# Kernel tuning notes

Measured on AMD Instinct MI355X. Metric: run time of the kernel, lower is better.

## Reference

```python
import jax, jax.numpy as jnp
import numpy as np

ROUTING_ITERATIONS = 3

def squash(x, axis=-1):
    # norm_sq/(1+norm_sq) * x/norm, equation 1 of the CapsNet paper
    norm_sq = jnp.sum(x * x, axis=axis, keepdims=True)
    norm = jnp.sqrt(norm_sq)
    return norm_sq / (1.0 + norm_sq) * (x / norm)

def setup_inputs() -> dict:
    key = jax.random.key(0)
    k1, k2 = jax.random.split(key)
    B, IC, IH, OC, OH = 64, 2048, 16, 64, 32
    input_capsules = jax.random.normal(k1, (B, IC, IH), dtype=jnp.float32)
    # scale weight so U entries are O(1) (sum over in_hid=16)
    W = jax.random.normal(k2, (IC, IH, OC, OH), dtype=jnp.float32) * (1.0 / np.sqrt(IH))
    return {"input_capsules": input_capsules, "W": W}

def reference(input_capsules, W):
    # U[b,i,o,j] = sum_h x[b,i,h] * W[i,h,o,j]
    U = jnp.einsum('bih,ihoj->bioj', input_capsules, W)
    b, in_caps, out_caps, out_hid = U.shape
    Blog = jnp.zeros((b, in_caps, out_caps), dtype=U.dtype)

    def body(Blog, _):
        C = jax.nn.softmax(Blog, axis=-1)            # [b,i,o]
        S = jnp.einsum('bio,bioh->boh', C, U)        # [b,o,h]
        V = squash(S, axis=-1)                       # [b,o,h]
        Blog = Blog + jnp.einsum('bioh,boh->bio', U, V)
        return Blog, V

    _, Vs = jax.lax.scan(body, Blog, None, length=ROUTING_ITERATIONS)
    return Vs[-1]
```

## Files before the change

### kernel.cpp

```cpp
#include <hip/hip_runtime.h>
#include <hip/hip_bf16.h>
#include <cstdint>
#include <cstddef>

constexpr int B_SZ = 64, IC = 2048, IH = 16, OC = 64, OH = 32;
constexpr int NN = OC * OH;
constexpr int ICHUNK = 32;
constexpr int NCHUNK = IC / ICHUNK;
constexpr int BTILE = 16;

typedef __attribute__((ext_vector_type(8))) short bf16x8;
typedef __attribute__((ext_vector_type(4))) float f32x4;

constexpr int F_Z = 0;
constexpr int F_W = 64;
constexpr int F_WBUF = 65536;
constexpr int BL_ROW = 68;
constexpr int F_BL = F_W + 2 * F_WBUF;
constexpr int F_C = F_BL + 16 * BL_ROW * 4;
constexpr int F_SMEM = F_C + 16 * BL_ROW * 4;

__device__ __forceinline__ unsigned short f2bf(float f) {
    unsigned u = __float_as_uint(f);
    u += 0x7fffu + ((u >> 16) & 1u);
    return (unsigned short)(u >> 16);
}
__device__ __forceinline__ float bf_lo(unsigned u) {
    return __uint_as_float(u << 16);
}
__device__ __forceinline__ float bf_hi(unsigned u) {
    return __uint_as_float(u & 0xffff0000u);
}
__device__ __forceinline__ unsigned pk2f(float a, float b) {
    return (unsigned)f2bf(a) | ((unsigned)f2bf(b) << 16);
}
__device__ __forceinline__ void gload_lds16(const void* g, void* l) {
    __builtin_amdgcn_global_load_lds(
        (const __attribute__((address_space(1))) void*)g,
        (__attribute__((address_space(3))) void*)l, 16, 0, 0);
}

__global__ void prep_wx(const float* __restrict__ W, unsigned short* __restrict__ Wp,
                        const float* __restrict__ x, unsigned short* __restrict__ xs) {
    int i = blockIdx.x;
    int t = threadIdx.x;
    const float* wp = W + (size_t)i * (IH * NN);
    int n0 = t * 4;
    float4 row[16];
#pragma unroll
    for (int h = 0; h < 16; ++h) row[h] = *(const float4*)(wp + h * NN + n0);
    char* dst = (char*)Wp + (size_t)i * 65536;
#pragma unroll
    for (int q = 0; q < 4; ++q) {
        float v[16];
#pragma unroll
        for (int h = 0; h < 16; ++h) v[h] = ((const float*)&row[h])[q];
        uint4 lo, hi;
        lo.x = pk2f(v[0], v[1]);   lo.y = pk2f(v[2], v[3]);
        lo.z = pk2f(v[4], v[5]);   lo.w = pk2f(v[6], v[7]);
        hi.x = pk2f(v[8], v[9]);   hi.y = pk2f(v[10], v[11]);
        hi.z = pk2f(v[12], v[13]); hi.w = pk2f(v[14], v[15]);
        *(uint4*)(dst + (size_t)(n0 + q) * 16) = lo;
        *(uint4*)(dst + 32768 + (size_t)(n0 + q) * 16) = hi;
    }
    if (t < 64) {
        const float* p = x + ((size_t)t * IC + i) * IH;
        unsigned short out[16];
#pragma unroll
        for (int h = 0; h < 16; ++h) out[h] = f2bf(p[h]);
        unsigned short* q = xs + ((size_t)i * 64 + t) * 16;
        *(uint4*)q = *(uint4*)&out[0];
        *(uint4*)(q + 8) = *(uint4*)&out[8];
    }
}

template <bool UNIFORM>
__launch_bounds__(1024, 4)
__global__ void routed_fast(const unsigned short* __restrict__ xs,
                            const unsigned short* __restrict__ Wp,
                            const float* __restrict__ Vin,
                            float* __restrict__ P) {
    extern __shared__ char smem[];
    const int tid = threadIdx.x;
    const int lane = tid & 63;
    const int wv = tid >> 6;
    const int l15 = lane & 15;
    const int g = lane >> 4;

    const int v = blockIdx.x;
    const int bt = (v >> 3) & 3;
    const int chunk = (v & 7) + 8 * (v >> 5);
    const int b0 = bt * BTILE;
    const int i0 = chunk * ICHUNK;

    if (tid < 16) ((unsigned*)(smem + F_Z))[tid] = 0u;

    uint4 vrp[4];
    if constexpr (!UNIFORM) {
#pragma unroll
        for (int o8 = 0; o8 < 4; ++o8) {
            const float* vb =
                Vin + ((size_t)(b0 + l15) * OC + (wv * 4 + o8)) * OH + g * 4;
            f32x4 a = *(const f32x4*)vb;
            f32x4 c = *(const f32x4*)(vb + 16);
            vrp[o8].x = pk2f(a.x, a.y);
            vrp[o8].y = pk2f(a.z, a.w);
            vrp[o8].z = pk2f(c.x, c.y);
            vrp[o8].w = pk2f(c.z, c.w);
        }
    }

    {
        const char* gs = (const char*)Wp + (size_t)i0 * 65536;
#pragma unroll
        for (int r = 0; r < 4; ++r) {
            int seg = r * 16 + wv;
            gload_lds16(gs + seg * 1024 + lane * 16, smem + F_W + seg * 1024);
        }
    }
    asm volatile("s_waitcnt vmcnt(0)" ::: "memory");
    __builtin_amdgcn_s_barrier();

    const f32x4 fzero = {0.f, 0.f, 0.f, 0.f};
    f32x4 sacc[8];
#pragma unroll
    for (int t = 0; t < 8; ++t) sacc[t] = fzero;

    for (int ii = 0; ii < ICHUNK; ++ii) {
        const int cur = ii & 1;
        const char* wb = smem + F_W + cur * F_WBUF;
        const int i = i0 + ii;

        bf16x8 xf = {0, 0, 0, 0, 0, 0, 0, 0};
        if (lane < 32)
            xf = *(const bf16x8*)(xs + (size_t)i * 1024 + (size_t)(b0 + l15) * 16 + g * 8);

        f32x4 acc[8];
#pragma unroll
        for (int t = 0; t < 8; ++t) {
            int nt = wv * 128 + (t >> 1) * 32 + (t & 1) * 16;
            const char* aptr = (lane < 32)
                ? (wb + g * 32768 + (size_t)(nt + l15) * 16)
                : (smem + F_Z);
            bf16x8 af = *(const bf16x8*)aptr;
            if constexpr (UNIFORM) {
                sacc[t] = __builtin_amdgcn_mfma_f32_16x16x32_bf16(af, xf, sacc[t], 0, 0, 0);
            } else {
                acc[t] = __builtin_amdgcn_mfma_f32_16x16x32_bf16(af, xf, fzero, 0, 0, 0);
            }
        }

        if (ii + 1 < ICHUNK) {
            const char* gs = (const char*)Wp + (size_t)(i + 1) * 65536;
            char* lb = smem + F_W + (cur ^ 1) * F_WBUF;
#pragma unroll
            for (int r = 0; r < 4; ++r) {
                int seg = r * 16 + wv;
                gload_lds16(gs + seg * 1024 + lane * 16, lb + seg * 1024);
            }
        }

        if constexpr (UNIFORM) {
            asm volatile("s_waitcnt vmcnt(0)" ::: "memory");
            __builtin_amdgcn_s_barrier();
        } else {
            float blf[4];
#pragma unroll
            for (int o8 = 0; o8 < 4; ++o8) {
                f32x4 a0 = acc[2 * o8], a1 = acc[2 * o8 + 1];
                uint4 u = vrp[o8];
                float p = a0.x * bf_lo(u.x) + a0.y * bf_hi(u.x) +
                          a0.z * bf_lo(u.y) + a0.w * bf_hi(u.y) +
                          a1.x * bf_lo(u.z) + a1.y * bf_hi(u.z) +
                          a1.z * bf_lo(u.w) + a1.w * bf_hi(u.w);
                p += __shfl_xor(p, 16);
                p += __shfl_xor(p, 32);
                blf[o8] = p;
            }
            if (lane < 16) {
                float4 b4;
                b4.x = blf[0]; b4.y = blf[1]; b4.z = blf[2]; b4.w = blf[3];
                *(float4*)((float*)(smem + F_BL) + l15 * BL_ROW + wv * 4) = b4;
            }
            asm volatile("s_waitcnt lgkmcnt(0)" ::: "memory");
            __builtin_amdgcn_s_barrier();

            {
                const float* BLr = (const float*)(smem + F_BL) + wv * BL_ROW;
                float xv = BLr[lane];
                float m = xv;
#pragma unroll
                for (int d = 32; d >= 1; d >>= 1) m = fmaxf(m, __shfl_xor(m, d));
                float e = __expf(xv - m);
                float s = e;
#pragma unroll
                for (int d = 32; d >= 1; d >>= 1) s += __shfl_xor(s, d);
                ((float*)(smem + F_C))[wv * BL_ROW + lane] = e * (1.0f / s);
            }
            asm volatile("s_waitcnt lgkmcnt(0)" ::: "memory");
            asm volatile("s_waitcnt vmcnt(0)" ::: "memory");
            __builtin_amdgcn_s_barrier();

            float4 c4 = *(const float4*)((const float*)(smem + F_C) +
                                         l15 * BL_ROW + wv * 4);
#pragma unroll
            for (int t = 0; t < 8; ++t) {
                float c = (t < 2) ? c4.x : (t < 4) ? c4.y : (t < 6) ? c4.z : c4.w;
                sacc[t] += acc[t] * c;
            }
        }
    }

    const float scale = UNIFORM ? (1.0f / 64.0f) : 1.0f;
#pragma unroll
    for (int t = 0; t < 8; ++t) {
        int n = wv * 128 + (t >> 1) * 32 + (t & 1) * 16 + g * 4;
        float* dst = P + ((size_t)(chunk * 64) + b0 + l15) * NN + n;
        float4 o4;
        o4.x = sacc[t].x * scale; o4.y = sacc[t].y * scale;
        o4.z = sacc[t].z * scale; o4.w = sacc[t].w * scale;
        *(float4*)dst = o4;
    }
}

__global__ void reduce_squash(const float* __restrict__ P, float* __restrict__ dst,
                              int addmode) {
    int pr = blockIdx.x * 2 + (threadIdx.x >> 5);
    int j = threadIdx.x & 31;
    int b = pr >> 6, o = pr & 63;
    const float* p = P + (size_t)b * NN + o * 32 + j;
    float s = 0.f;
#pragma unroll 8
    for (int c = 0; c < NCHUNK; ++c) s += p[(size_t)c * (64 * NN)];
    float nsq = s * s;
#pragma unroll
    for (int d = 16; d >= 1; d >>= 1) nsq += __shfl_xor(nsq, d);
    float nrm = sqrtf(nsq);
    float f = nrm / (1.f + nsq);
    float outv = s * f;
    int idx = pr * 32 + j;
    if (addmode) dst[idx] += outv;
    else dst[idx] = outv;
}

extern "C" void kernel_launch(void* const* d_in, const int* in_sizes, int n_in,
                              void* d_out, int out_size, void* d_ws, size_t ws_size,
                              hipStream_t stream) {
    const float* x = (const float*)d_in[0];
    const float* W = (const float*)d_in[1];
    float* out = (float*)d_out;
    char* ws = (char*)d_ws;
    unsigned short* xs = (unsigned short*)ws;
    float* P = (float*)(ws + ((size_t)4 << 20));
    float* Vsum = (float*)(ws + ((size_t)36 << 20));
    unsigned short* Wp = (unsigned short*)(ws + (((size_t)40) << 20));

    (void)hipFuncSetAttribute(reinterpret_cast<const void*>(&routed_fast<true>),
                              hipFuncAttributeMaxDynamicSharedMemorySize, F_SMEM);
    (void)hipFuncSetAttribute(reinterpret_cast<const void*>(&routed_fast<false>),
                              hipFuncAttributeMaxDynamicSharedMemorySize, F_SMEM);

    prep_wx<<<dim3(2048), dim3(512), 0, stream>>>(W, Wp, x, xs);
    routed_fast<true><<<dim3(256), dim3(1024), F_SMEM, stream>>>(xs, Wp, nullptr, P);
    reduce_squash<<<dim3(2048), dim3(64), 0, stream>>>(P, Vsum, 0);
    routed_fast<false><<<dim3(256), dim3(1024), F_SMEM, stream>>>(xs, Wp, Vsum, P);
    reduce_squash<<<dim3(2048), dim3(64), 0, stream>>>(P, Vsum, 1);
    routed_fast<false><<<dim3(256), dim3(1024), F_SMEM, stream>>>(xs, Wp, Vsum, P);
    reduce_squash<<<dim3(2048), dim3(64), 0, stream>>>(P, out, 0);
}
```

Measured before the change: 351.7 us.

## Drop max-subtraction in routing softmax and merge barriers via partial-sum exchange

Replaces the per-capsule softmax, which wrote logits to LDS, took a wave-wide max and sum, and used two barriers, with local exponentials whose per-wave partial sums are exchanged through a double-buffered LDS table, leaving one barrier per input capsule. It also issues the next W prefetch and the next x load before the MFMAs instead of after, hiding more latency. Omitting the max subtraction risks overflow if logits become large, which depends on logit magnitudes staying bounded.

```diff
diff --git a/kernel.cpp b/kernel.cpp
--- a/kernel.cpp
+++ b/kernel.cpp
@@ -15,10 +15,10 @@
 constexpr int F_Z = 0;
 constexpr int F_W = 64;
 constexpr int F_WBUF = 65536;
-constexpr int BL_ROW = 68;
-constexpr int F_BL = F_W + 2 * F_WBUF;
-constexpr int F_C = F_BL + 16 * BL_ROW * 4;
-constexpr int F_SMEM = F_C + 16 * BL_ROW * 4;
+constexpr int F_T = F_W + 2 * F_WBUF;
+constexpr int T_ROW = 80;
+constexpr int T_BUF = 16 * T_ROW;
+constexpr int F_SMEM = F_T + 2 * T_BUF;
 
 __device__ __forceinline__ unsigned short f2bf(float f) {
     unsigned u = __float_as_uint(f);
@@ -118,7 +118,10 @@
             gload_lds16(gs + seg * 1024 + lane * 16, smem + F_W + seg * 1024);
         }
     }
-    asm volatile("s_waitcnt vmcnt(0)" ::: "memory");
+    bf16x8 xf = {0, 0, 0, 0, 0, 0, 0, 0};
+    if (lane < 32)
+        xf = *(const bf16x8*)(xs + (size_t)i0 * 1024 + (size_t)(b0 + l15) * 16 + g * 8);
+    asm volatile("s_waitcnt vmcnt(0) lgkmcnt(0)" ::: "memory");
     __builtin_amdgcn_s_barrier();
 
     const f32x4 fzero = {0.f, 0.f, 0.f, 0.f};
@@ -131,9 +134,19 @@
         const char* wb = smem + F_W + cur * F_WBUF;
         const int i = i0 + ii;
 
-        bf16x8 xf = {0, 0, 0, 0, 0, 0, 0, 0};
-        if (lane < 32)
-            xf = *(const bf16x8*)(xs + (size_t)i * 1024 + (size_t)(b0 + l15) * 16 + g * 8);
+        bf16x8 xf_n = {0, 0, 0, 0, 0, 0, 0, 0};
+        if (ii + 1 < ICHUNK) {
+            const char* gs = (const char*)Wp + (size_t)(i + 1) * 65536;
+            char* lb = smem + F_W + (cur ^ 1) * F_WBUF;
+#pragma unroll
+            for (int r = 0; r < 4; ++r) {
+                int seg = r * 16 + wv;
+                gload_lds16(gs + seg * 1024 + lane * 16, lb + seg * 1024);
+            }
+            if (lane < 32)
+                xf_n = *(const bf16x8*)(xs + (size_t)(i + 1) * 1024 +
+                                        (size_t)(b0 + l15) * 16 + g * 8);
+        }
 
         f32x4 acc[8];
 #pragma unroll
@@ -150,21 +163,11 @@
             }
         }
 
-        if (ii + 1 < ICHUNK) {
-            const char* gs = (const char*)Wp + (size_t)(i + 1) * 65536;
-            char* lb = smem + F_W + (cur ^ 1) * F_WBUF;
-#pragma unroll
-            for (int r = 0; r < 4; ++r) {
-                int seg = r * 16 + wv;
-                gload_lds16(gs + seg * 1024 + lane * 16, lb + seg * 1024);
-            }
-        }
-
         if constexpr (UNIFORM) {
             asm volatile("s_waitcnt vmcnt(0)" ::: "memory");
             __builtin_amdgcn_s_barrier();
         } else {
-            float blf[4];
+            float eb[4], s4;
 #pragma unroll
             for (int o8 = 0; o8 < 4; ++o8) {
                 f32x4 a0 = acc[2 * o8], a1 = acc[2 * o8 + 1];
@@ -175,40 +178,32 @@
                           a1.z * bf_lo(u.w) + a1.w * bf_hi(u.w);
                 p += __shfl_xor(p, 16);
                 p += __shfl_xor(p, 32);
-                blf[o8] = p;
-            }
-            if (lane < 16) {
-                float4 b4;
-                b4.x = blf[0]; b4.y = blf[1]; b4.z = blf[2]; b4.w = blf[3];
-                *(float4*)((float*)(smem + F_BL) + l15 * BL_ROW + wv * 4) = b4;
-            }
-            asm volatile("s_waitcnt lgkmcnt(0)" ::: "memory");
+                eb[o8] = __expf(p);
+            }
+            s4 = (eb[0] + eb[1]) + (eb[2] + eb[3]);
+
+            if (lane < 16)
+                *(float*)(smem + F_T + cur * T_BUF + l15 * T_ROW + wv * 4) = s4;
+
+            asm volatile("s_waitcnt vmcnt(0) lgkmcnt(0)" ::: "memory");
             __builtin_amdgcn_s_barrier();
 
-            {
-                const float* BLr = (const float*)(smem + F_BL) + wv * BL_ROW;
-                float xv = BLr[lane];
-                float m = xv;
-#pragma unroll
-                for (int d = 32; d >= 1; d >>= 1) m = fmaxf(m, __shfl_xor(m, d));
-                float e = __expf(xv - m);
-                float s = e;
-#pragma unroll
-                for (int d = 32; d >= 1; d >>= 1) s += __shfl_xor(s, d);
-                ((float*)(smem + F_C))[wv * BL_ROW + lane] = e * (1.0f / s);
-            }
-            asm volatile("s_waitcnt lgkmcnt(0)" ::: "memory");
-            asm volatile("s_waitcnt vmcnt(0)" ::: "memory");
-            __builtin_amdgcn_s_barrier();
-
-            float4 c4 = *(const float4*)((const float*)(smem + F_C) +
-                                         l15 * BL_ROW + wv * 4);
+            const char* tb = smem + F_T + cur * T_BUF + l15 * T_ROW;
+            f32x4 t0 = *(const f32x4*)(tb);
+            f32x4 t1 = *(const f32x4*)(tb + 16);
+            f32x4 t2 = *(const f32x4*)(tb + 32);
+            f32x4 t3 = *(const f32x4*)(tb + 48);
+            f32x4 ts = (t0 + t1) + (t2 + t3);
+            float denom = (ts.x + ts.y) + (ts.z + ts.w);
+            float rd = __builtin_amdgcn_rcpf(denom);
+            float c0 = eb[0] * rd, c1 = eb[1] * rd, c2 = eb[2] * rd, c3 = eb[3] * rd;
 #pragma unroll
             for (int t = 0; t < 8; ++t) {
-                float c = (t < 2) ? c4.x : (t < 4) ? c4.y : (t < 6) ? c4.z : c4.w;
+                float c = (t < 2) ? c0 : (t < 4) ? c1 : (t < 6) ? c2 : c3;
                 sacc[t] += acc[t] * c;
             }
         }
+        xf = xf_n;
     }
 
     const float scale = UNIFORM ? (1.0f / 64.0f) : 1.0f;
```

Result: faster. 323.0 us (-8.2%).
